# Kernel tuning notes

Measured on AMD Instinct MI355X. Metric: run time of the kernel, lower is better.

The kernel has to match this reference:

```python
import jax, jax.numpy as jnp
import numpy as np

NEG_SLOPE = 0.2  # PyG GATConv default leaky_relu slope
EPS = 1e-16      # PyG softmax denominator epsilon


def gat_conv(x, src, dst, W, a_src, a_dst, num_nodes):
    """Single-head PyG GATConv (concat=True, heads=1, no bias), self-loops already in src/dst."""
    h = x @ W                                  # [N, out]
    alpha_src = h @ a_src                      # [N]
    alpha_dst = h @ a_dst                      # [N]
    e = jax.nn.leaky_relu(alpha_src[src] + alpha_dst[dst], NEG_SLOPE)  # [E]
    # segment softmax over destination nodes
    m = jax.ops.segment_max(e, dst, num_segments=num_nodes)           # [N]
    ex = jnp.exp(e - m[dst])                                          # [E]
    denom = jax.ops.segment_sum(ex, dst, num_segments=num_nodes)      # [N]
    alpha = ex / (denom[dst] + EPS)                                   # [E]
    # scatter-add weighted source features to destinations
    out = jax.ops.segment_sum(h[src] * alpha[:, None], dst, num_segments=num_nodes)
    return out


def setup_inputs() -> dict:
    key = jax.random.key(0)
    N, E, F_in, H, C = 100000, 1600000, 256, 64, 40
    ks = jax.random.split(key, 12)
    x = jax.random.normal(ks[0], (N, F_in), dtype=jnp.float32)
    edge_index = jax.random.randint(ks[1], (2, E), 0, N, dtype=jnp.int64)
    s = 0.1
    return {
        "x": x,
        "edge_index": edge_index,
        "W0": jax.random.normal(ks[2], (F_in, H), dtype=jnp.float32) * s,
        "asrc0": jax.random.normal(ks[3], (H,), dtype=jnp.float32) * s,
        "adst0": jax.random.normal(ks[4], (H,), dtype=jnp.float32) * s,
        "W1": jax.random.normal(ks[5], (H, H), dtype=jnp.float32) * s,
        "asrc1": jax.random.normal(ks[6], (H,), dtype=jnp.float32) * s,
        "adst1": jax.random.normal(ks[7], (H,), dtype=jnp.float32) * s,
        "W2": jax.random.normal(ks[8], (H, C), dtype=jnp.float32) * s,
        "asrc2": jax.random.normal(ks[9], (C,), dtype=jnp.float32) * s,
        "adst2": jax.random.normal(ks[10], (C,), dtype=jnp.float32) * s,
    }


def reference(x, edge_index, W0, asrc0, adst0, W1, asrc1, adst1, W2, asrc2, adst2):
    N = x.shape[0]
    # PyG GATConv add_self_loops=True: append (i, i) for every node
    loops = jnp.arange(N, dtype=edge_index.dtype)
    src = jnp.concatenate([edge_index[0], loops])
    dst = jnp.concatenate([edge_index[1], loops])
    params = [(W0, asrc0, adst0), (W1, asrc1, adst1), (W2, asrc2, adst2)]
    h = x
    for i, (W, a_s, a_d) in enumerate(params):
        h = gat_conv(h, src, dst, W, a_s, a_d, N)
        # type_norm='None' -> batch_norm is identity; eval mode -> no dropout/side losses
        if i != len(params) - 1:
            h = jax.nn.relu(h)
    return h
```

## Files before the change

### kernel.cpp

```cpp
#include <hip/hip_runtime.h>
#include <hip/hip_fp16.h>

#define CAP 56
#define BINW 128
#define CAPB 2560
#define CHUNK 4096
#define NEG_SLOPE 0.2f

typedef _Float16 f16x8 __attribute__((ext_vector_type(8)));
typedef float    f32x4 __attribute__((ext_vector_type(4)));

__global__ void k_initcur(int* __restrict__ gcur, int nbin) {
    int i = blockIdx.x * blockDim.x + threadIdx.x;
    if (i < nbin) gcur[i] = i * CAPB;
}

__global__ __launch_bounds__(256) void k_bin(const int* __restrict__ esrc,
                                             const int* __restrict__ edst,
                                             int E, int N, int nbin,
                                             int* __restrict__ gcur,
                                             int* __restrict__ binbuf) {
    __shared__ int hist[1024];
    __shared__ int base[1024];

    const int tid = threadIdx.x;
    const int tot = E + N;
    const int start = blockIdx.x * CHUNK;
    const int end = (start + CHUNK < tot) ? start + CHUNK : tot;

    for (int i = tid; i < nbin; i += 256) hist[i] = 0;
    __syncthreads();

    for (int i = start + tid; i < end; i += 256) {
        int d = (i < E) ? edst[i] : (i - E);
        atomicAdd(&hist[d >> 7], 1);
    }
    __syncthreads();

    for (int i = tid; i < nbin; i += 256) {
        int h = hist[i];
        base[i] = h ? atomicAdd(&gcur[i], h) : 0;
    }
    __syncthreads();
    for (int i = tid; i < nbin; i += 256) hist[i] = 0;
    __syncthreads();

    for (int i = start + tid; i < end; i += 256) {
        int s, d;
        if (i < E) { s = esrc[i]; d = edst[i]; }
        else       { s = i - E;   d = s; }
        int b = d >> 7;
        int p = base[b] + atomicAdd(&hist[b], 1);
        if (p < (b + 1) * CAPB)
            binbuf[p] = ((d & (BINW - 1)) << 17) | s;
    }
}

__global__ __launch_bounds__(256) void k_bucket_bin(const int* __restrict__ binbuf,
                                                    const int* __restrict__ gcur,
                                                    int N,
                                                    int* __restrict__ cnt,
                                                    int* __restrict__ bucket) {
    __shared__ int lcnt[BINW];
    __shared__ int lb[BINW * CAP];

    const int tid = threadIdx.x;
    const int b = blockIdx.x;

    int n = gcur[b] - b * CAPB;
    if (n > CAPB) n = CAPB;

    for (int i = tid; i < BINW; i += 256) lcnt[i] = 0;
    for (int i = tid; i < BINW * CAP; i += 256) lb[i] = 0;
    __syncthreads();

    const int* src = binbuf + (size_t)b * CAPB;
    for (int i = tid; i < n; i += 256) {
        int x = src[i];
        int s = x & 0x1ffff;
        int dl = x >> 17;
        int p = atomicAdd(&lcnt[dl], 1);
        if (p < CAP) lb[dl * CAP + p] = s;
    }
    __syncthreads();

    size_t gbase = (size_t)b * BINW * CAP;
    for (int i = tid; i < BINW * CAP; i += 256)
        bucket[gbase + i] = lb[i];
    for (int i = tid; i < BINW; i += 256) {
        int v = b * BINW + i;
        if (v < N) cnt[v] = (lcnt[i] < CAP) ? lcnt[i] : CAP;
    }
}

template <int K, int FR>
__global__ __launch_bounds__(256, 4) void k_gemm_mfma(const float* __restrict__ X,
                                                      const float* __restrict__ W,
                                                      const float* __restrict__ a_s,
                                                      const float* __restrict__ a_d,
                                                      __half* __restrict__ H16,
                                                      float* __restrict__ AS,
                                                      float* __restrict__ AD,
                                                      int N) {
    constexpr int NSTEP = K / 32;
    constexpr int G = K / 8;
    constexpr int SCR = 76;
    constexpr size_t WT_B  = (size_t)64 * K * 2;
    constexpr size_t SCR_B = (size_t)4 * 32 * SCR * 2;

    __shared__ __align__(16) char smem[(WT_B > SCR_B) ? WT_B : SCR_B];
    _Float16* Wt = (_Float16*)smem;

    const int tid  = threadIdx.x;
    const int wid  = tid >> 6;
    const int lane = tid & 63;
    const int lrow = lane & 15;
    const int g    = lane >> 4;
    const int row0 = blockIdx.x * 128 + wid * 32;

    for (int i = tid; i < K * 64; i += 256) {
        int k = i >> 6, c = i & 63;
        float w = (c < FR) ? W[(size_t)k * FR + c] : 0.f;
        int gr = (k >> 3) ^ (c & (G - 1));
        Wt[c * K + gr * 8 + (k & 7)] = (_Float16)w;
    }
    __syncthreads();

    f32x4 acc[2][4];
#pragma unroll
    for (int rf = 0; rf < 2; ++rf)
#pragma unroll
        for (int cf = 0; cf < 4; ++cf) {
            f32x4 z = {0.f, 0.f, 0.f, 0.f};
            acc[rf][cf] = z;
        }

    int r0 = row0 + lrow;      if (r0 > N - 1) r0 = N - 1;
    int r1 = row0 + 16 + lrow; if (r1 > N - 1) r1 = N - 1;
    const float* xp0 = X + (size_t)r0 * K + g * 8;
    const float* xp1 = X + (size_t)r1 * K + g * 8;

    float4 c0  = *reinterpret_cast<const float4*>(xp0);
    float4 c0b = *reinterpret_cast<const float4*>(xp0 + 4);
    float4 c1  = *reinterpret_cast<const float4*>(xp1);
    float4 c1b = *reinterpret_cast<const float4*>(xp1 + 4);

#pragma unroll
    for (int ks = 0; ks < NSTEP; ++ks) {
        float4 n0, n0b, n1, n1b;
        if (ks + 1 < NSTEP) {
            n0  = *reinterpret_cast<const float4*>(xp0 + (ks + 1) * 32);
            n0b = *reinterpret_cast<const float4*>(xp0 + (ks + 1) * 32 + 4);
            n1  = *reinterpret_cast<const float4*>(xp1 + (ks + 1) * 32);
            n1b = *reinterpret_cast<const float4*>(xp1 + (ks + 1) * 32 + 4);
        }

        f16x8 b[4];
#pragma unroll
        for (int cf = 0; cf < 4; ++cf) {
            int c = cf * 16 + lrow;
            int t = ks * 4 + g;
            b[cf] = *reinterpret_cast<const f16x8*>(
                &Wt[c * K + ((t ^ (c & (G - 1))) << 3)]);
        }

        float fa0[8] = {c0.x, c0.y, c0.z, c0.w, c0b.x, c0b.y, c0b.z, c0b.w};
        float fa1[8] = {c1.x, c1.y, c1.z, c1.w, c1b.x, c1b.y, c1b.z, c1b.w};
        f16x8 h0, l0, h1, l1;
#pragma unroll
        for (int j = 0; j < 8; ++j) {
            _Float16 hv0 = (_Float16)fa0[j];
            h0[j] = hv0; l0[j] = (_Float16)(fa0[j] - (float)hv0);
            _Float16 hv1 = (_Float16)fa1[j];
            h1[j] = hv1; l1[j] = (_Float16)(fa1[j] - (float)hv1);
        }

#pragma unroll
        for (int cf = 0; cf < 4; ++cf) {
            acc[0][cf] = __builtin_amdgcn_mfma_f32_16x16x32_f16(h0, b[cf], acc[0][cf], 0, 0, 0);
            acc[0][cf] = __builtin_amdgcn_mfma_f32_16x16x32_f16(l0, b[cf], acc[0][cf], 0, 0, 0);
            acc[1][cf] = __builtin_amdgcn_mfma_f32_16x16x32_f16(h1, b[cf], acc[1][cf], 0, 0, 0);
            acc[1][cf] = __builtin_amdgcn_mfma_f32_16x16x32_f16(l1, b[cf], acc[1][cf], 0, 0, 0);
        }

        c0 = n0; c0b = n0b; c1 = n1; c1b = n1b;
    }

#pragma unroll
    for (int rf = 0; rf < 2; ++rf) {
        float ss[4] = {0.f, 0.f, 0.f, 0.f}, sd[4] = {0.f, 0.f, 0.f, 0.f};
#pragma unroll
        for (int cf = 0; cf < 4; ++cf) {
            int c = cf * 16 + lrow;
            float va = (c < FR) ? a_s[c] : 0.f;
            float vd = (c < FR) ? a_d[c] : 0.f;
#pragma unroll
            for (int q = 0; q < 4; ++q) {
                ss[q] = fmaf(acc[rf][cf][q], va, ss[q]);
                sd[q] = fmaf(acc[rf][cf][q], vd, sd[q]);
            }
        }
#pragma unroll
        for (int off = 1; off < 16; off <<= 1) {
#pragma unroll
            for (int q = 0; q < 4; ++q) {
                ss[q] += __shfl_xor(ss[q], off);
                sd[q] += __shfl_xor(sd[q], off);
            }
        }
        if (lrow == 0) {
#pragma unroll
            for (int q = 0; q < 4; ++q) {
                int r = row0 + rf * 16 + g * 4 + q;
                if (r < N) { AS[r] = ss[q]; AD[r] = sd[q]; }
            }
        }
    }

    __syncthreads();
    _Float16* scr = (_Float16*)smem + (size_t)wid * 32 * SCR;

#pragma unroll
    for (int rf = 0; rf < 2; ++rf)
#pragma unroll
        for (int cf = 0; cf < 4; ++cf)
#pragma unroll
            for (int q = 0; q < 4; ++q)
                scr[(rf * 16 + g * 4 + q) * SCR + cf * 16 + lrow] =
                    (_Float16)acc[rf][cf][q];

    int sr = lane >> 1, half = lane & 1;
    int grow = row0 + sr;
    if (grow < N) {
#pragma unroll
        for (int q = 0; q < 4; ++q) {
            f16x8 v = *reinterpret_cast<const f16x8*>(
                &scr[sr * SCR + half * 32 + q * 8]);
            *reinterpret_cast<f16x8*>(&H16[(size_t)grow * 64 + half * 32 + q * 8]) = v;
        }
    }
}

template <int FR>
__global__ __launch_bounds__(256) void k_gemm_mfma_h(const __half* __restrict__ A16,
                                                     const float* __restrict__ W,
                                                     const float* __restrict__ a_s,
                                                     const float* __restrict__ a_d,
                                                     __half* __restrict__ H16,
                                                     float* __restrict__ AS,
                                                     float* __restrict__ AD,
                                                     int N) {
    constexpr int K = 64;
    constexpr int G = K / 8;
    constexpr int SCR = 76;
    constexpr size_t WT_B  = (size_t)64 * K * 2;
    constexpr size_t SCR_B = (size_t)4 * 32 * SCR * 2;

    __shared__ __align__(16) char smem[(WT_B > SCR_B) ? WT_B : SCR_B];
    _Float16* Wt = (_Float16*)smem;

    const int tid  = threadIdx.x;
    const int wid  = tid >> 6;
    const int lane = tid & 63;
    const int lrow = lane & 15;
    const int g    = lane >> 4;
    const int row0 = blockIdx.x * 128 + wid * 32;

    for (int i = tid; i < K * 64; i += 256) {
        int k = i >> 6, c = i & 63;
        float w = (c < FR) ? W[(size_t)k * FR + c] : 0.f;
        int gr = (k >> 3) ^ (c & (G - 1));
        Wt[c * K + gr * 8 + (k & 7)] = (_Float16)w;
    }
    __syncthreads();

    f32x4 acc[2][4];
#pragma unroll
    for (int rf = 0; rf < 2; ++rf)
#pragma unroll
        for (int cf = 0; cf < 4; ++cf) {
            f32x4 z = {0.f, 0.f, 0.f, 0.f};
            acc[rf][cf] = z;
        }

    int r0 = row0 + lrow;      if (r0 > N - 1) r0 = N - 1;
    int r1 = row0 + 16 + lrow; if (r1 > N - 1) r1 = N - 1;
    const _Float16* ap0 = (const _Float16*)A16 + (size_t)r0 * K + g * 8;
    const _Float16* ap1 = (const _Float16*)A16 + (size_t)r1 * K + g * 8;

#pragma unroll
    for (int ks = 0; ks < 2; ++ks) {
        f16x8 a0 = *reinterpret_cast<const f16x8*>(ap0 + ks * 32);
        f16x8 a1 = *reinterpret_cast<const f16x8*>(ap1 + ks * 32);

        f16x8 b[4];
#pragma unroll
        for (int cf = 0; cf < 4; ++cf) {
            int c = cf * 16 + lrow;
            int t = ks * 4 + g;
            b[cf] = *reinterpret_cast<const f16x8*>(
                &Wt[c * K + ((t ^ (c & (G - 1))) << 3)]);
        }

#pragma unroll
        for (int cf = 0; cf < 4; ++cf) {
            acc[0][cf] = __builtin_amdgcn_mfma_f32_16x16x32_f16(a0, b[cf], acc[0][cf], 0, 0, 0);
            acc[1][cf] = __builtin_amdgcn_mfma_f32_16x16x32_f16(a1, b[cf], acc[1][cf], 0, 0, 0);
        }
    }

#pragma unroll
    for (int rf = 0; rf < 2; ++rf) {
        float ss[4] = {0.f, 0.f, 0.f, 0.f}, sd[4] = {0.f, 0.f, 0.f, 0.f};
#pragma unroll
        for (int cf = 0; cf < 4; ++cf) {
            int c = cf * 16 + lrow;
            float va = (c < FR) ? a_s[c] : 0.f;
            float vd = (c < FR) ? a_d[c] : 0.f;
#pragma unroll
            for (int q = 0; q < 4; ++q) {
                ss[q] = fmaf(acc[rf][cf][q], va, ss[q]);
                sd[q] = fmaf(acc[rf][cf][q], vd, sd[q]);
            }
        }
#pragma unroll
        for (int off = 1; off < 16; off <<= 1) {
#pragma unroll
            for (int q = 0; q < 4; ++q) {
                ss[q] += __shfl_xor(ss[q], off);
                sd[q] += __shfl_xor(sd[q], off);
            }
        }
        if (lrow == 0) {
#pragma unroll
            for (int q = 0; q < 4; ++q) {
                int r = row0 + rf * 16 + g * 4 + q;
                if (r < N) { AS[r] = ss[q]; AD[r] = sd[q]; }
            }
        }
    }

    __syncthreads();
    _Float16* scr = (_Float16*)smem + (size_t)wid * 32 * SCR;

#pragma unroll
    for (int rf = 0; rf < 2; ++rf)
#pragma unroll
        for (int cf = 0; cf < 4; ++cf)
#pragma unroll
            for (int q = 0; q < 4; ++q)
                scr[(rf * 16 + g * 4 + q) * SCR + cf * 16 + lrow] =
                    (_Float16)acc[rf][cf][q];

    if (FR == 64) {
        int sr = lane >> 1, half = lane & 1;
        int grow = row0 + sr;
        if (grow < N) {
#pragma unroll
            for (int q = 0; q < 4; ++q) {
                f16x8 v = *reinterpret_cast<const f16x8*>(
                    &scr[sr * SCR + half * 32 + q * 8]);
                *reinterpret_cast<f16x8*>(&H16[(size_t)grow * 64 + half * 32 + q * 8]) = v;
            }
        }
    } else {
        constexpr int CH = FR / 8;
        for (int idx = lane; idx < 32 * CH; idx += 64) {
            int sr = idx / CH, c8 = idx % CH;
            int grow = row0 + sr;
            if (grow < N) {
                f16x8 v = *reinterpret_cast<const f16x8*>(
                    &scr[sr * SCR + c8 * 8]);
                *reinterpret_cast<f16x8*>(&H16[(size_t)grow * FR + c8 * 8]) = v;
            }
        }
    }
}

template <int F, bool RELU, bool OUT16>
__global__ __launch_bounds__(256) void k_aggregate2(const __half* __restrict__ H16,
                                                    const float* __restrict__ AS,
                                                    const float* __restrict__ AD,
                                                    const int* __restrict__ cnt,
                                                    const int* __restrict__ bucket,
                                                    void* __restrict__ OUT,
                                                    int N) {
    const int hw = (blockIdx.x * blockDim.x + threadIdx.x) >> 5;
    const int l  = threadIdx.x & 31;
    if (hw >= N) return;
    const int v = hw;

    int deg = cnt[v];
    int s0 = -1, s1 = -1;
    if (l < deg)      s0 = bucket[(size_t)v * CAP + l];
    if (32 + l < deg) s1 = bucket[(size_t)v * CAP + 32 + l];

    float adv = AD[v];
    float e0 = -3.4e38f, e1 = -3.4e38f;
    if (s0 >= 0) { float t = AS[s0] + adv; e0 = (t > 0.f) ? t : NEG_SLOPE * t; }
    if (s1 >= 0) { float t = AS[s1] + adv; e1 = (t > 0.f) ? t : NEG_SLOPE * t; }

    float m = fmaxf(e0, e1);
#pragma unroll
    for (int off = 16; off; off >>= 1) m = fmaxf(m, __shfl_xor(m, off, 32));

    float x0 = (s0 >= 0) ? __expf(e0 - m) : 0.f;
    float x1 = (s1 >= 0) ? __expf(e1 - m) : 0.f;

    float dsum = x0 + x1;
#pragma unroll
    for (int off = 16; off; off >>= 1) dsum += __shfl_xor(dsum, off, 32);

    float inv = 1.f / (dsum + 1e-16f);

    const bool act = (2 * l) < F;
    const __half2* Hp = reinterpret_cast<const __half2*>(H16);
    constexpr int F2 = F / 2;

    float ax0 = 0.f, ay0 = 0.f, ax1 = 0.f, ay1 = 0.f;
    float ax2 = 0.f, ay2 = 0.f, ax3 = 0.f, ay3 = 0.f;

    int dA = (deg < 32) ? deg : 32;
    int dB = deg - dA;

    int e = 0;
    for (; e + 4 <= dA; e += 4) {
        int   se0 = __shfl(s0, e, 32),     se1 = __shfl(s0, e + 1, 32);
        int   se2 = __shfl(s0, e + 2, 32), se3 = __shfl(s0, e + 3, 32);
        float w0  = __shfl(x0, e, 32),     w1  = __shfl(x0, e + 1, 32);
        float w2  = __shfl(x0, e + 2, 32), w3  = __shfl(x0, e + 3, 32);
        if (act) {
            float2 h0 = __half22float2(Hp[(size_t)se0 * F2 + l]);
            float2 h1 = __half22float2(Hp[(size_t)se1 * F2 + l]);
            float2 h2 = __half22float2(Hp[(size_t)se2 * F2 + l]);
            float2 h3 = __half22float2(Hp[(size_t)se3 * F2 + l]);
            ax0 = fmaf(h0.x, w0, ax0); ay0 = fmaf(h0.y, w0, ay0);
            ax1 = fmaf(h1.x, w1, ax1); ay1 = fmaf(h1.y, w1, ay1);
            ax2 = fmaf(h2.x, w2, ax2); ay2 = fmaf(h2.y, w2, ay2);
            ax3 = fmaf(h3.x, w3, ax3); ay3 = fmaf(h3.y, w3, ay3);
        }
    }
    for (; e < dA; ++e) {
        int   se = __shfl(s0, e, 32);
        float we = __shfl(x0, e, 32);
        if (act) {
            float2 h = __half22float2(Hp[(size_t)se * F2 + l]);
            ax0 = fmaf(h.x, we, ax0); ay0 = fmaf(h.y, we, ay0);
        }
    }
    e = 0;
    for (; e + 4 <= dB; e += 4) {
        int   se0 = __shfl(s1, e, 32),     se1 = __shfl(s1, e + 1, 32);
        int   se2 = __shfl(s1, e + 2, 32), se3 = __shfl(s1, e + 3, 32);
        float w0  = __shfl(x1, e, 32),     w1  = __shfl(x1, e + 1, 32);
        float w2  = __shfl(x1, e + 2, 32), w3  = __shfl(x1, e + 3, 32);
        if (act) {
            float2 h0 = __half22float2(Hp[(size_t)se0 * F2 + l]);
            float2 h1 = __half22float2(Hp[(size_t)se1 * F2 + l]);
            float2 h2 = __half22float2(Hp[(size_t)se2 * F2 + l]);
            float2 h3 = __half22float2(Hp[(size_t)se3 * F2 + l]);
            ax0 = fmaf(h0.x, w0, ax0); ay0 = fmaf(h0.y, w0, ay0);
            ax1 = fmaf(h1.x, w1, ax1); ay1 = fmaf(h1.y, w1, ay1);
            ax2 = fmaf(h2.x, w2, ax2); ay2 = fmaf(h2.y, w2, ay2);
            ax3 = fmaf(h3.x, w3, ax3); ay3 = fmaf(h3.y, w3, ay3);
        }
    }
    for (; e < dB; ++e) {
        int   se = __shfl(s1, e, 32);
        float we = __shfl(x1, e, 32);
        if (act) {
            float2 h = __half22float2(Hp[(size_t)se * F2 + l]);
            ax0 = fmaf(h.x, we, ax0); ay0 = fmaf(h.y, we, ay0);
        }
    }

    float fx = ((ax0 + ax1) + (ax2 + ax3)) * inv;
    float fy = ((ay0 + ay1) + (ay2 + ay3)) * inv;
    if (RELU) { fx = fmaxf(fx, 0.f); fy = fmaxf(fy, 0.f); }

    if (act) {
        if (OUT16) {
            ((__half2*)OUT)[(size_t)v * F2 + l] = __floats2half2_rn(fx, fy);
        } else {
            *reinterpret_cast<float2*>(&((float*)OUT)[(size_t)v * F + 2 * l]) =
                make_float2(fx, fy);
        }
    }
}

extern "C" void kernel_launch(void* const* d_in, const int* in_sizes, int n_in,
                              void* d_out, int out_size, void* d_ws, size_t ws_size,
                              hipStream_t stream) {
    const float* x     = (const float*)d_in[0];
    const int*   ei    = (const int*)d_in[1];
    const float* W0    = (const float*)d_in[2];
    const float* asrc0 = (const float*)d_in[3];
    const float* adst0 = (const float*)d_in[4];
    const float* W1    = (const float*)d_in[5];
    const float* asrc1 = (const float*)d_in[6];
    const float* adst1 = (const float*)d_in[7];
    const float* W2    = (const float*)d_in[8];
    const float* asrc2 = (const float*)d_in[9];
    const float* adst2 = (const float*)d_in[10];

    const int F_IN = 256, H_DIM = 64;
    int N = in_sizes[0] / F_IN;
    int E = in_sizes[1] / 2;
    int nbin = (N + BINW - 1) / BINW;

    const int* esrc = ei;
    const int* edst = ei + E;

    char* w = (char*)d_ws;
    __half* h16    = (__half*)w; w += (size_t)N * H_DIM * 2;
    __half* agg16  = (__half*)w; w += (size_t)N * H_DIM * 2;
    float*  AS     = (float*)w;  w += (size_t)N * 4;
    float*  AD     = (float*)w;  w += (size_t)N * 4;
    int*    cnt    = (int*)w;    w += (size_t)N * 4;
    int*    bucket = (int*)w;    w += (size_t)nbin * BINW * CAP * 4;
    int*    binbuf = (int*)w;    w += (size_t)nbin * CAPB * 4;
    int*    gcur   = (int*)w;    w += (size_t)nbin * 4;

    float* out = (float*)d_out;

    k_initcur<<<(nbin + 255) / 256, 256, 0, stream>>>(gcur, nbin);
    {
        int tot = E + N;
        int blocks = (tot + CHUNK - 1) / CHUNK;
        k_bin<<<blocks, 256, 0, stream>>>(esrc, edst, E, N, nbin, gcur, binbuf);
    }
    k_bucket_bin<<<nbin, 256, 0, stream>>>(binbuf, gcur, N, cnt, bucket);

    int gb  = (N + 127) / 128;
    int ab2 = (N + 7) / 8;

    k_gemm_mfma<256, 64><<<gb, 256, 0, stream>>>(x, W0, asrc0, adst0, h16, AS, AD, N);
    k_aggregate2<64, true, true><<<ab2, 256, 0, stream>>>(h16, AS, AD, cnt, bucket, agg16, N);

    k_gemm_mfma_h<64><<<gb, 256, 0, stream>>>(agg16, W1, asrc1, adst1, h16, AS, AD, N);
    k_aggregate2<64, true, true><<<ab2, 256, 0, stream>>>(h16, AS, AD, cnt, bucket, agg16, N);

    k_gemm_mfma_h<40><<<gb, 256, 0, stream>>>(agg16, W2, asrc2, adst2, h16, AS, AD, N);
    k_aggregate2<40, false, false><<<ab2, 256, 0, stream>>>(h16, AS, AD, cnt, bucket, out, N);
}
```

Baseline: 404.0 us.

## Halve GEMM row tiles, deepen X prefetch, and unroll aggregation gathers by eight

The GEMM kernels now give each wave 16 rows instead of 32 and launch twice as many blocks. The first-layer GEMM keeps a 4-deep register ring of X loads in flight, and the hidden-layer GEMM gets a higher occupancy hint. The aggregation loop now gathers 8 neighbour rows per iteration into 8 separate accumulators instead of 4, to expose more memory-level parallelism on the random gathers. In exchange, each block reloads W into shared memory more often relative to the rows it processes, and register pressure may rise.

```diff
diff --git a/kernel.cpp b/kernel.cpp
--- a/kernel.cpp
+++ b/kernel.cpp
@@ -93,7 +93,7 @@
     }
 }
 
-template <int K, int FR>
+template <int K>
 __global__ __launch_bounds__(256, 4) void k_gemm_mfma(const float* __restrict__ X,
                                                       const float* __restrict__ W,
                                                       const float* __restrict__ a_s,
@@ -104,9 +104,9 @@
                                                       int N) {
     constexpr int NSTEP = K / 32;
     constexpr int G = K / 8;
-    constexpr int SCR = 76;
+    constexpr int SCR = 80;
     constexpr size_t WT_B  = (size_t)64 * K * 2;
-    constexpr size_t SCR_B = (size_t)4 * 32 * SCR * 2;
+    constexpr size_t SCR_B = (size_t)4 * 16 * SCR * 2;
 
     __shared__ __align__(16) char smem[(WT_B > SCR_B) ? WT_B : SCR_B];
     _Float16* Wt = (_Float16*)smem;
@@ -116,7 +116,138 @@
     const int lane = tid & 63;
     const int lrow = lane & 15;
     const int g    = lane >> 4;
-    const int row0 = blockIdx.x * 128 + wid * 32;
+    const int row0 = blockIdx.x * 64 + wid * 16;
+
+    for (int i = tid; i < K * 64; i += 256) {
+        int k = i >> 6, c = i & 63;
+        float w = W[(size_t)k * 64 + c];
+        int gr = (k >> 3) ^ (c & (G - 1));
+        Wt[c * K + gr * 8 + (k & 7)] = (_Float16)w;
+    }
+    __syncthreads();
+
+    f32x4 acc[4];
+#pragma unroll
+    for (int cf = 0; cf < 4; ++cf) {
+        f32x4 z = {0.f, 0.f, 0.f, 0.f};
+        acc[cf] = z;
+    }
+
+    int r = row0 + lrow; if (r > N - 1) r = N - 1;
+    const float* xp = X + (size_t)r * K + g * 8;
+
+    float4 bA[4], bB[4];
+#pragma unroll
+    for (int p = 0; p < 4; ++p) {
+        bA[p] = *reinterpret_cast<const float4*>(xp + p * 32);
+        bB[p] = *reinterpret_cast<const float4*>(xp + p * 32 + 4);
+    }
+
+#pragma unroll
+    for (int ks = 0; ks < NSTEP; ++ks) {
+        f16x8 b[4];
+#pragma unroll
+        for (int cf = 0; cf < 4; ++cf) {
+            int c = cf * 16 + lrow;
+            int t = ks * 4 + g;
+            b[cf] = *reinterpret_cast<const f16x8*>(
+                &Wt[c * K + ((t ^ (c & (G - 1))) << 3)]);
+        }
+
+        float fa[8] = {bA[ks & 3].x, bA[ks & 3].y, bA[ks & 3].z, bA[ks & 3].w,
+                       bB[ks & 3].x, bB[ks & 3].y, bB[ks & 3].z, bB[ks & 3].w};
+        f16x8 hi, lo;
+#pragma unroll
+        for (int j = 0; j < 8; ++j) {
+            _Float16 hv = (_Float16)fa[j];
+            hi[j] = hv; lo[j] = (_Float16)(fa[j] - (float)hv);
+        }
+
+        if (ks + 4 < NSTEP) {
+            bA[ks & 3] = *reinterpret_cast<const float4*>(xp + (ks + 4) * 32);
+            bB[ks & 3] = *reinterpret_cast<const float4*>(xp + (ks + 4) * 32 + 4);
+        }
+
+#pragma unroll
+        for (int cf = 0; cf < 4; ++cf) {
+            acc[cf] = __builtin_amdgcn_mfma_f32_16x16x32_f16(hi, b[cf], acc[cf], 0, 0, 0);
+            acc[cf] = __builtin_amdgcn_mfma_f32_16x16x32_f16(lo, b[cf], acc[cf], 0, 0, 0);
+        }
+    }
+
+    {
+        float ss[4] = {0.f, 0.f, 0.f, 0.f}, sd[4] = {0.f, 0.f, 0.f, 0.f};
+#pragma unroll
+        for (int cf = 0; cf < 4; ++cf) {
+            int c = cf * 16 + lrow;
+            float va = a_s[c];
+            float vd = a_d[c];
+#pragma unroll
+            for (int q = 0; q < 4; ++q) {
+                ss[q] = fmaf(acc[cf][q], va, ss[q]);
+                sd[q] = fmaf(acc[cf][q], vd, sd[q]);
+            }
+        }
+#pragma unroll
+        for (int off = 1; off < 16; off <<= 1) {
+#pragma unroll
+            for (int q = 0; q < 4; ++q) {
+                ss[q] += __shfl_xor(ss[q], off);
+                sd[q] += __shfl_xor(sd[q], off);
+            }
+        }
+        if (lrow == 0) {
+#pragma unroll
+            for (int q = 0; q < 4; ++q) {
+                int rr = row0 + g * 4 + q;
+                if (rr < N) { AS[rr] = ss[q]; AD[rr] = sd[q]; }
+            }
+        }
+    }
+
+    __syncthreads();
+    _Float16* scr = (_Float16*)smem + (size_t)wid * 16 * SCR;
+
+#pragma unroll
+    for (int cf = 0; cf < 4; ++cf)
+#pragma unroll
+        for (int q = 0; q < 4; ++q)
+            scr[(g * 4 + q) * SCR + cf * 16 + lrow] = (_Float16)acc[cf][q];
+
+    int sr = lane >> 2, seg = lane & 3;
+    int grow = row0 + sr;
+    if (grow < N) {
+        f16x8 v0 = *reinterpret_cast<const f16x8*>(&scr[sr * SCR + seg * 16]);
+        f16x8 v1 = *reinterpret_cast<const f16x8*>(&scr[sr * SCR + seg * 16 + 8]);
+        *reinterpret_cast<f16x8*>(&H16[(size_t)grow * 64 + seg * 16]) = v0;
+        *reinterpret_cast<f16x8*>(&H16[(size_t)grow * 64 + seg * 16 + 8]) = v1;
+    }
+}
+
+template <int FR>
+__global__ __launch_bounds__(256, 6) void k_gemm_mfma_h(const __half* __restrict__ A16,
+                                                        const float* __restrict__ W,
+                                                        const float* __restrict__ a_s,
+                                                        const float* __restrict__ a_d,
+                                                        __half* __restrict__ H16,
+                                                        float* __restrict__ AS,
+                                                        float* __restrict__ AD,
+                                                        int N) {
+    constexpr int K = 64;
+    constexpr int G = K / 8;
+    constexpr int SCR = 80;
+    constexpr size_t WT_B  = (size_t)64 * K * 2;
+    constexpr size_t SCR_B = (size_t)4 * 16 * SCR * 2;
+
+    __shared__ __align__(16) char smem[(WT_B > SCR_B) ? WT_B : SCR_B];
+    _Float16* Wt = (_Float16*)smem;
+
+    const int tid  = threadIdx.x;
+    const int wid  = tid >> 6;
+    const int lane = tid & 63;
+    const int lrow = lane & 15;
+    const int g    = lane >> 4;
+    const int row0 = blockIdx.x * 64 + wid * 16;
 
     for (int i = tid; i < K * 64; i += 256) {
         int k = i >> 6, c = i & 63;
@@ -126,35 +257,21 @@
     }
     __syncthreads();
 
-    f32x4 acc[2][4];
-#pragma unroll
-    for (int rf = 0; rf < 2; ++rf)
-#pragma unroll
-        for (int cf = 0; cf < 4; ++cf) {
-            f32x4 z = {0.f, 0.f, 0.f, 0.f};
-            acc[rf][cf] = z;
-        }
-
-    int r0 = row0 + lrow;      if (r0 > N - 1) r0 = N - 1;
-    int r1 = row0 + 16 + lrow; if (r1 > N - 1) r1 = N - 1;
-    const float* xp0 = X + (size_t)r0 * K + g * 8;
-    const float* xp1 = X + (size_t)r1 * K + g * 8;
-
-    float4 c0  = *reinterpret_cast<const float4*>(xp0);
-    float4 c0b = *reinterpret_cast<const float4*>(xp0 + 4);
-    float4 c1  = *reinterpret_cast<const float4*>(xp1);
-    float4 c1b = *reinterpret_cast<const float4*>(xp1 + 4);
-
-#pragma unroll
-    for (int ks = 0; ks < NSTEP; ++ks) {
-        float4 n0, n0b, n1, n1b;
-        if (ks + 1 < NSTEP) {
-            n0  = *reinterpret_cast<const float4*>(xp0 + (ks + 1) * 32);
-            n0b = *reinterpret_cast<const float4*>(xp0 + (ks + 1) * 32 + 4);
-            n1  = *reinterpret_cast<const float4*>(xp1 + (ks + 1) * 32);
-            n1b = *reinterpret_cast<const float4*>(xp1 + (ks + 1) * 32 + 4);
-        }
-
+    f32x4 acc[4];
+#pragma unroll
+    for (int cf = 0; cf < 4; ++cf) {
+        f32x4 z = {0.f, 0.f, 0.f, 0.f};
+        acc[cf] = z;
+    }
+
+    int r = row0 + lrow; if (r > N - 1) r = N - 1;
+    const _Float16* ap = (const _Float16*)A16 + (size_t)r * K + g * 8;
+
+    f16x8 a0 = *reinterpret_cast<const f16x8*>(ap);
+    f16x8 a1 = *reinterpret_cast<const f16x8*>(ap + 32);
+
+#pragma unroll
+    for (int ks = 0; ks < 2; ++ks) {
         f16x8 b[4];
 #pragma unroll
         for (int cf = 0; cf < 4; ++cf) {
@@ -163,31 +280,13 @@
             b[cf] = *reinterpret_cast<const f16x8*>(
                 &Wt[c * K + ((t ^ (c & (G - 1))) << 3)]);
         }
-
-        float fa0[8] = {c0.x, c0.y, c0.z, c0.w, c0b.x, c0b.y, c0b.z, c0b.w};
-        float fa1[8] = {c1.x, c1.y, c1.z, c1.w, c1b.x, c1b.y, c1b.z, c1b.w};
-        f16x8 h0, l0, h1, l1;
-#pragma unroll
-        for (int j = 0; j < 8; ++j) {
-            _Float16 hv0 = (_Float16)fa0[j];
-            h0[j] = hv0; l0[j] = (_Float16)(fa0[j] - (float)hv0);
-            _Float16 hv1 = (_Float16)fa1[j];
-            h1[j] = hv1; l1[j] = (_Float16)(fa1[j] - (float)hv1);
-        }
-
-#pragma unroll
-        for (int cf = 0; cf < 4; ++cf) {
-            acc[0][cf] = __builtin_amdgcn_mfma_f32_16x16x32_f16(h0, b[cf], acc[0][cf], 0, 0, 0);
-            acc[0][cf] = __builtin_amdgcn_mfma_f32_16x16x32_f16(l0, b[cf], acc[0][cf], 0, 0, 0);
-            acc[1][cf] = __builtin_amdgcn_mfma_f32_16x16x32_f16(h1, b[cf], acc[1][cf], 0, 0, 0);
-            acc[1][cf] = __builtin_amdgcn_mfma_f32_16x16x32_f16(l1, b[cf], acc[1][cf], 0, 0, 0);
-        }
-
-        c0 = n0; c0b = n0b; c1 = n1; c1b = n1b;
-    }
-
-#pragma unroll
-    for (int rf = 0; rf < 2; ++rf) {
+        f16x8 a = (ks == 0) ? a0 : a1;
+#pragma unroll
+        for (int cf = 0; cf < 4; ++cf)
+            acc[cf] = __builtin_amdgcn_mfma_f32_16x16x32_f16(a, b[cf], acc[cf], 0, 0, 0);
+    }
+
+    {
         float ss[4] = {0.f, 0.f, 0.f, 0.f}, sd[4] = {0.f, 0.f, 0.f, 0.f};
 #pragma unroll
         for (int cf = 0; cf < 4; ++cf) {
@@ -196,8 +295,8 @@
             float vd = (c < FR) ? a_d[c] : 0.f;
 #pragma unroll
             for (int q = 0; q < 4; ++q) {
-                ss[q] = fmaf(acc[rf][cf][q], va, ss[q]);
-                sd[q] = fmaf(acc[rf][cf][q], vd, sd[q]);
+                ss[q] = fmaf(acc[cf][q], va, ss[q]);
+                sd[q] = fmaf(acc[cf][q], vd, sd[q]);
             }
         }
 #pragma unroll
@@ -211,166 +310,37 @@
         if (lrow == 0) {
 #pragma unroll
             for (int q = 0; q < 4; ++q) {
-                int r = row0 + rf * 16 + g * 4 + q;
-                if (r < N) { AS[r] = ss[q]; AD[r] = sd[q]; }
-            }
-        }
-    }
-
-    __syncthreads();
-    _Float16* scr = (_Float16*)smem + (size_t)wid * 32 * SCR;
-
-#pragma unroll
-    for (int rf = 0; rf < 2; ++rf)
-#pragma unroll
-        for (int cf = 0; cf < 4; ++cf)
-#pragma unroll
-            for (int q = 0; q < 4; ++q)
-                scr[(rf * 16 + g * 4 + q) * SCR + cf * 16 + lrow] =
-                    (_Float16)acc[rf][cf][q];
-
-    int sr = lane >> 1, half = lane & 1;
-    int grow = row0 + sr;
-    if (grow < N) {
-#pragma unroll
-        for (int q = 0; q < 4; ++q) {
-            f16x8 v = *reinterpret_cast<const f16x8*>(
-                &scr[sr * SCR + half * 32 + q * 8]);
-            *reinterpret_cast<f16x8*>(&H16[(size_t)grow * 64 + half * 32 + q * 8]) = v;
-        }
-    }
-}
-
-template <int FR>
-__global__ __launch_bounds__(256) void k_gemm_mfma_h(const __half* __restrict__ A16,
-                                                     const float* __restrict__ W,
-                                                     const float* __restrict__ a_s,
-                                                     const float* __restrict__ a_d,
-                                                     __half* __restrict__ H16,
-                                                     float* __restrict__ AS,
-                                                     float* __restrict__ AD,
-                                                     int N) {
-    constexpr int K = 64;
-    constexpr int G = K / 8;
-    constexpr int SCR = 76;
-    constexpr size_t WT_B  = (size_t)64 * K * 2;
-    constexpr size_t SCR_B = (size_t)4 * 32 * SCR * 2;
-
-    __shared__ __align__(16) char smem[(WT_B > SCR_B) ? WT_B : SCR_B];
-    _Float16* Wt = (_Float16*)smem;
-
-    const int tid  = threadIdx.x;
-    const int wid  = tid >> 6;
-    const int lane = tid & 63;
-    const int lrow = lane & 15;
-    const int g    = lane >> 4;
-    const int row0 = blockIdx.x * 128 + wid * 32;
-
-    for (int i = tid; i < K * 64; i += 256) {
-        int k = i >> 6, c = i & 63;
-        float w = (c < FR) ? W[(size_t)k * FR + c] : 0.f;
-        int gr = (k >> 3) ^ (c & (G - 1));
-        Wt[c * K + gr * 8 + (k & 7)] = (_Float16)w;
-    }
-    __syncthreads();
-
-    f32x4 acc[2][4];
-#pragma unroll
-    for (int rf = 0; rf < 2; ++rf)
-#pragma unroll
-        for (int cf = 0; cf < 4; ++cf) {
-            f32x4 z = {0.f, 0.f, 0.f, 0.f};
-            acc[rf][cf] = z;
-        }
-
-    int r0 = row0 + lrow;      if (r0 > N - 1) r0 = N - 1;
-    int r1 = row0 + 16 + lrow; if (r1 > N - 1) r1 = N - 1;
-    const _Float16* ap0 = (const _Float16*)A16 + (size_t)r0 * K + g * 8;
-    const _Float16* ap1 = (const _Float16*)A16 + (size_t)r1 * K + g * 8;
-
-#pragma unroll
-    for (int ks = 0; ks < 2; ++ks) {
-        f16x8 a0 = *reinterpret_cast<const f16x8*>(ap0 + ks * 32);
-        f16x8 a1 = *reinterpret_cast<const f16x8*>(ap1 + ks * 32);
-
-        f16x8 b[4];
-#pragma unroll
-        for (int cf = 0; cf < 4; ++cf) {
-            int c = cf * 16 + lrow;
-            int t = ks * 4 + g;
-            b[cf] = *reinterpret_cast<const f16x8*>(
-                &Wt[c * K + ((t ^ (c & (G - 1))) << 3)]);
-        }
-
-#pragma unroll
-        for (int cf = 0; cf < 4; ++cf) {
-            acc[0][cf] = __builtin_amdgcn_mfma_f32_16x16x32_f16(a0, b[cf], acc[0][cf], 0, 0, 0);
-            acc[1][cf] = __builtin_amdgcn_mfma_f32_16x16x32_f16(a1, b[cf], acc[1][cf], 0, 0, 0);
-        }
-    }
-
-#pragma unroll
-    for (int rf = 0; rf < 2; ++rf) {
-        float ss[4] = {0.f, 0.f, 0.f, 0.f}, sd[4] = {0.f, 0.f, 0.f, 0.f};
-#pragma unroll
-        for (int cf = 0; cf < 4; ++cf) {
-            int c = cf * 16 + lrow;
-            float va = (c < FR) ? a_s[c] : 0.f;
-            float vd = (c < FR) ? a_d[c] : 0.f;
-#pragma unroll
-            for (int q = 0; q < 4; ++q) {
-                ss[q] = fmaf(acc[rf][cf][q], va, ss[q]);
-                sd[q] = fmaf(acc[rf][cf][q], vd, sd[q]);
-            }
-        }
-#pragma unroll
-        for (int off = 1; off < 16; off <<= 1) {
-#pragma unroll
-            for (int q = 0; q < 4; ++q) {
-                ss[q] += __shfl_xor(ss[q], off);
-                sd[q] += __shfl_xor(sd[q], off);
-            }
-        }
-        if (lrow == 0) {
-#pragma unroll
-            for (int q = 0; q < 4; ++q) {
-                int r = row0 + rf * 16 + g * 4 + q;
-                if (r < N) { AS[r] = ss[q]; AD[r] = sd[q]; }
-            }
-        }
-    }
-
-    __syncthreads();
-    _Float16* scr = (_Float16*)smem + (size_t)wid * 32 * SCR;
-
-#pragma unroll
-    for (int rf = 0; rf < 2; ++rf)
-#pragma unroll
-        for (int cf = 0; cf < 4; ++cf)
-#pragma unroll
-            for (int q = 0; q < 4; ++q)
-                scr[(rf * 16 + g * 4 + q) * SCR + cf * 16 + lrow] =
-                    (_Float16)acc[rf][cf][q];
+                int rr = row0 + g * 4 + q;
+                if (rr < N) { AS[rr] = ss[q]; AD[rr] = sd[q]; }
+            }
+        }
+    }
+
+    __syncthreads();
+    _Float16* scr = (_Float16*)smem + (size_t)wid * 16 * SCR;
+
+#pragma unroll
+    for (int cf = 0; cf < 4; ++cf)
+#pragma unroll
+        for (int q = 0; q < 4; ++q)
+            scr[(g * 4 + q) * SCR + cf * 16 + lrow] = (_Float16)acc[cf][q];
 
     if (FR == 64) {
-        int sr = lane >> 1, half = lane & 1;
+        int sr = lane >> 2, seg = lane & 3;
         int grow = row0 + sr;
         if (grow < N) {
-#pragma unroll
-            for (int q = 0; q < 4; ++q) {
-                f16x8 v = *reinterpret_cast<const f16x8*>(
-                    &scr[sr * SCR + half * 32 + q * 8]);
-                *reinterpret_cast<f16x8*>(&H16[(size_t)grow * 64 + half * 32 + q * 8]) = v;
-            }
+            f16x8 v0 = *reinterpret_cast<const f16x8*>(&scr[sr * SCR + seg * 16]);
+            f16x8 v1 = *reinterpret_cast<const f16x8*>(&scr[sr * SCR + seg * 16 + 8]);
+            *reinterpret_cast<f16x8*>(&H16[(size_t)grow * 64 + seg * 16]) = v0;
+            *reinterpret_cast<f16x8*>(&H16[(size_t)grow * 64 + seg * 16 + 8]) = v1;
         }
     } else {
         constexpr int CH = FR / 8;
-        for (int idx = lane; idx < 32 * CH; idx += 64) {
+        for (int idx = lane; idx < 16 * CH; idx += 64) {
             int sr = idx / CH, c8 = idx % CH;
             int grow = row0 + sr;
             if (grow < N) {
-                f16x8 v = *reinterpret_cast<const f16x8*>(
-                    &scr[sr * SCR + c8 * 8]);
+                f16x8 v = *reinterpret_cast<const f16x8*>(&scr[sr * SCR + c8 * 8]);
                 *reinterpret_cast<f16x8*>(&H16[(size_t)grow * FR + c8 * 8]) = v;
             }
         }
@@ -417,27 +387,28 @@
     const __half2* Hp = reinterpret_cast<const __half2*>(H16);
     constexpr int F2 = F / 2;
 
-    float ax0 = 0.f, ay0 = 0.f, ax1 = 0.f, ay1 = 0.f;
-    float ax2 = 0.f, ay2 = 0.f, ax3 = 0.f, ay3 = 0.f;
+    float ax[8] = {0.f,0.f,0.f,0.f,0.f,0.f,0.f,0.f};
+    float ay[8] = {0.f,0.f,0.f,0.f,0.f,0.f,0.f,0.f};
 
     int dA = (deg < 32) ? deg : 32;
     int dB = deg - dA;
 
     int e = 0;
-    for (; e + 4 <= dA; e += 4) {
-        int   se0 = __shfl(s0, e, 32),     se1 = __shfl(s0, e + 1, 32);
-        int   se2 = __shfl(s0, e + 2, 32), se3 = __shfl(s0, e + 3, 32);
-        float w0  = __shfl(x0, e, 32),     w1  = __shfl(x0, e + 1, 32);
-        float w2  = __shfl(x0, e + 2, 32), w3  = __shfl(x0, e + 3, 32);
+    for (; e + 8 <= dA; e += 8) {
+        int   se[8]; float we[8]; float2 h[8];
+#pragma unroll
+        for (int j = 0; j < 8; ++j) {
+            se[j] = __shfl(s0, e + j, 32);
+            we[j] = __shfl(x0, e + j, 32);
+        }
         if (act) {
-            float2 h0 = __half22float2(Hp[(size_t)se0 * F2 + l]);
-            float2 h1 = __half22float2(Hp[(size_t)se1 * F2 + l]);
-            float2 h2 = __half22float2(Hp[(size_t)se2 * F2 + l]);
-            float2 h3 = __half22float2(Hp[(size_t)se3 * F2 + l]);
-            ax0 = fmaf(h0.x, w0, ax0); ay0 = fmaf(h0.y, w0, ay0);
-            ax1 = fmaf(h1.x, w1, ax1); ay1 = fmaf(h1.y, w1, ay1);
-            ax2 = fmaf(h2.x, w2, ax2); ay2 = fmaf(h2.y, w2, ay2);
-            ax3 = fmaf(h3.x, w3, ax3); ay3 = fmaf(h3.y, w3, ay3);
+#pragma unroll
+            for (int j = 0; j < 8; ++j) h[j] = __half22float2(Hp[(size_t)se[j] * F2 + l]);
+#pragma unroll
+            for (int j = 0; j < 8; ++j) {
+                ax[j] = fmaf(h[j].x, we[j], ax[j]);
+                ay[j] = fmaf(h[j].y, we[j], ay[j]);
+            }
         }
     }
     for (; e < dA; ++e) {
@@ -445,24 +416,25 @@
         float we = __shfl(x0, e, 32);
         if (act) {
             float2 h = __half22float2(Hp[(size_t)se * F2 + l]);
-            ax0 = fmaf(h.x, we, ax0); ay0 = fmaf(h.y, we, ay0);
+            ax[0] = fmaf(h.x, we, ax[0]); ay[0] = fmaf(h.y, we, ay[0]);
         }
     }
     e = 0;
-    for (; e + 4 <= dB; e += 4) {
-        int   se0 = __shfl(s1, e, 32),     se1 = __shfl(s1, e + 1, 32);
-        int   se2 = __shfl(s1, e + 2, 32), se3 = __shfl(s1, e + 3, 32);
-        float w0  = __shfl(x1, e, 32),     w1  = __shfl(x1, e + 1, 32);
-        float w2  = __shfl(x1, e + 2, 32), w3  = __shfl(x1, e + 3, 32);
+    for (; e + 8 <= dB; e += 8) {
+        int   se[8]; float we[8]; float2 h[8];
+#pragma unroll
+        for (int j = 0; j < 8; ++j) {
+            se[j] = __shfl(s1, e + j, 32);
+            we[j] = __shfl(x1, e + j, 32);
+        }
         if (act) {
-            float2 h0 = __half22float2(Hp[(size_t)se0 * F2 + l]);
-            float2 h1 = __half22float2(Hp[(size_t)se1 * F2 + l]);
-            float2 h2 = __half22float2(Hp[(size_t)se2 * F2 + l]);
-            float2 h3 = __half22float2(Hp[(size_t)se3 * F2 + l]);
-            ax0 = fmaf(h0.x, w0, ax0); ay0 = fmaf(h0.y, w0, ay0);
-            ax1 = fmaf(h1.x, w1, ax1); ay1 = fmaf(h1.y, w1, ay1);
-            ax2 = fmaf(h2.x, w2, ax2); ay2 = fmaf(h2.y, w2, ay2);
-            ax3 = fmaf(h3.x, w3, ax3); ay3 = fmaf(h3.y, w3, ay3);
+#pragma unroll
+            for (int j = 0; j < 8; ++j) h[j] = __half22float2(Hp[(size_t)se[j] * F2 + l]);
+#pragma unroll
+            for (int j = 0; j < 8; ++j) {
+                ax[j] = fmaf(h[j].x, we[j], ax[j]);
+                ay[j] = fmaf(h[j].y, we[j], ay[j]);
+            }
         }
     }
     for (; e < dB; ++e) {
@@ -470,12 +442,12 @@
         float we = __shfl(x1, e, 32);
         if (act) {
             float2 h = __half22float2(Hp[(size_t)se * F2 + l]);
-            ax0 = fmaf(h.x, we, ax0); ay0 = fmaf(h.y, we, ay0);
-        }
-    }
-
-    float fx = ((ax0 + ax1) + (ax2 + ax3)) * inv;
-    float fy = ((ay0 + ay1) + (ay2 + ay3)) * inv;
+            ax[0] = fmaf(h.x, we, ax[0]); ay[0] = fmaf(h.y, we, ay[0]);
+        }
+    }
+
+    float fx = (((ax[0] + ax[1]) + (ax[2] + ax[3])) + ((ax[4] + ax[5]) + (ax[6] + ax[7]))) * inv;
+    float fy = (((ay[0] + ay[1]) + (ay[2] + ay[3])) + ((ay[4] + ay[5]) + (ay[6] + ay[7]))) * inv;
     if (RELU) { fx = fmaxf(fx, 0.f); fy = fmaxf(fy, 0.f); }
 
     if (act) {
@@ -531,10 +503,10 @@
     }
     k_bucket_bin<<<nbin, 256, 0, stream>>>(binbuf, gcur, N, cnt, bucket);
 
-    int gb  = (N + 127) / 128;
+    int gb  = (N + 63) / 64;
     int ab2 = (N + 7) / 8;
 
-    k_gemm_mfma<256, 64><<<gb, 256, 0, stream>>>(x, W0, asrc0, adst0, h16, AS, AD, N);
+    k_gemm_mfma<256><<<gb, 256, 0, stream>>>(x, W0, asrc0, adst0, h16, AS, AD, N);
     k_aggregate2<64, true, true><<<ab2, 256, 0, stream>>>(h16, AS, AD, cnt, bucket, agg16, N);
 
     k_gemm_mfma_h<64><<<gb, 256, 0, stream>>>(agg16, W1, asrc1, adst1, h16, AS, AD, N);
```

Result: no change. 400.1 us (-1.0%).
